# Optimization experiments

Measured on AMD Instinct MI355X. Metric: run time of the kernel, lower is better.

Reference implementation:

```python
import jax, jax.numpy as jnp
import numpy as np

NUM_INDUCING = 50
B = 1 << 20  # number of query states

Z_SCALE = jnp.array([0.25, 0.2, 0.08, 400.0, 10.0], dtype=jnp.float32)
Z_SHIFT = jnp.array([0.0, 0.0, 0.0, 800.0, 12.0], dtype=jnp.float32)


def setup_inputs() -> dict:
    key = jax.random.key(0)
    k1, k2 = jax.random.split(key)
    x_star = jax.random.normal(k1, (B, 5), dtype=jnp.float32)
    # learned params, faithful to the module's initializers
    log_lengthscale = jnp.log(jnp.array([0.2, 0.15, 0.1, 400.0, 15.0], dtype=jnp.float32))
    log_variance = jnp.asarray(jnp.log(0.08), dtype=jnp.float32)
    Z_raw = 0.5 * jax.random.normal(k2, (NUM_INDUCING, 5), dtype=jnp.float32)
    return {"x_star": x_star, "log_lengthscale": log_lengthscale,
            "log_variance": log_variance, "Z_raw": Z_raw}


def _matern52_from_d(d, prior_var):
    s = jnp.sqrt(5.0) * d
    return prior_var * (1.0 + s + (5.0 / 3.0) * d * d) * jnp.exp(-s)


def reference(x_star, log_lengthscale, log_variance, Z_raw):
    ls = jnp.exp(log_lengthscale)                      # (5,)
    prior_var = jnp.exp(log_variance)                  # scalar
    Z = jnp.tanh(Z_raw) * Z_SCALE + Z_SHIFT            # (M,5)
    inv_ls = 1.0 / (ls + 1e-8)
    Zs = Z * inv_ls                                    # scaled inducing pts (M,5)
    Xs = x_star * inv_ls                               # scaled queries (B,5)

    # K_ZZ: tiny (M,M), exact pairwise form
    diff = Zs[:, None, :] - Zs[None, :, :]             # (M,M,5)
    d_zz = jnp.sqrt(jnp.sum(diff * diff, axis=-1) + 1e-8)
    k_ZZ = _matern52_from_d(d_zz, prior_var)
    K_ZZ_inv = jnp.linalg.inv(k_ZZ + 1e-4 * jnp.eye(NUM_INDUCING, dtype=k_ZZ.dtype))

    # k_xZ: (B,M) via the GEMM-friendly expansion of squared distance
    x2 = jnp.sum(Xs * Xs, axis=-1)                     # (B,)
    z2 = jnp.sum(Zs * Zs, axis=-1)                     # (M,)
    d2 = x2[:, None] + z2[None, :] - 2.0 * (Xs @ Zs.T)  # (B,M)
    d_xz = jnp.sqrt(jnp.maximum(d2, 0.0) + 1e-8)
    k_xZ = _matern52_from_d(d_xz, prior_var)           # (B,M)

    red = jnp.einsum('bi,ij,bj->b', k_xZ, K_ZZ_inv, k_xZ)
    variance = jnp.maximum(prior_var - red, 1e-6)
    return jnp.sqrt(variance)                          # (B,)
```

## Files before the change

kernel.cpp:

```cpp
#include <hip/hip_runtime.h>
#include <hip/hip_bf16.h>
#include <math.h>

#define M 50
#define SQRT5 2.2360679774997896f

typedef short  bf16x8 __attribute__((ext_vector_type(8)));
typedef float  f32x4v __attribute__((ext_vector_type(4)));

__constant__ float c_zscale[5] = {0.25f, 0.2f, 0.08f, 400.0f, 10.0f};
__constant__ float c_zshift[5] = {0.0f, 0.0f, 0.0f, 800.0f, 12.0f};

#if __has_builtin(__builtin_amdgcn_sqrtf)
__device__ __forceinline__ float fsqrt(float x) { return __builtin_amdgcn_sqrtf(x); }
#else
__device__ __forceinline__ float fsqrt(float x) { return sqrtf(x); }
#endif

#if __has_builtin(__builtin_amdgcn_exp2f)
__device__ __forceinline__ float fexp2(float x) { return __builtin_amdgcn_exp2f(x); }
#else
__device__ __forceinline__ float fexp2(float x) { return exp2f(x); }
#endif

__device__ __forceinline__ float lane_bcast(float v, int lane) {
    return __builtin_bit_cast(float,
        __builtin_amdgcn_readlane(__builtin_bit_cast(int, v), lane));
}

__device__ __forceinline__ unsigned short bfu(float f) {
    return __builtin_bit_cast(unsigned short, __float2bfloat16(f));
}

#define FOR50(F) F(0) F(1) F(2) F(3) F(4) F(5) F(6) F(7) F(8) F(9) \
  F(10) F(11) F(12) F(13) F(14) F(15) F(16) F(17) F(18) F(19) \
  F(20) F(21) F(22) F(23) F(24) F(25) F(26) F(27) F(28) F(29) \
  F(30) F(31) F(32) F(33) F(34) F(35) F(36) F(37) F(38) F(39) \
  F(40) F(41) F(42) F(43) F(44) F(45) F(46) F(47) F(48) F(49)
#define FOR50P(F, p) F(0,p) F(1,p) F(2,p) F(3,p) F(4,p) F(5,p) F(6,p) F(7,p) F(8,p) F(9,p) \
  F(10,p) F(11,p) F(12,p) F(13,p) F(14,p) F(15,p) F(16,p) F(17,p) F(18,p) F(19,p) \
  F(20,p) F(21,p) F(22,p) F(23,p) F(24,p) F(25,p) F(26,p) F(27,p) F(28,p) F(29,p) \
  F(30,p) F(31,p) F(32,p) F(33,p) F(34,p) F(35,p) F(36,p) F(37,p) F(38,p) F(39,p) \
  F(40,p) F(41,p) F(42,p) F(43,p) F(44,p) F(45,p) F(46,p) F(47,p) F(48,p) F(49,p)

#define DECL_R(i) float r##i;
#define INIT_R(i) r##i = s_K[(i) * M + jc];
#define UPD(i, p) if ((i) != (p)) { \
    const float cp = lane_bcast(r##i, (p)); \
    r##i = fmaf(-cp, rowv, onp ? 0.0f : r##i); }
#define PIVOT(p) { \
    const float piv  = lane_bcast(r##p, (p)); \
    const float ipv  = 1.0f / piv; \
    const bool  onp  = (j == (p)); \
    const float rowv = onp ? ipv : r##p * ipv; \
    FOR50P(UPD, p) \
    r##p = rowv; }
#define WB_R(i) s_K[(i) * M + j] = r##i;

#define DECL_C(i) float c##i;
#define INIT_C(i) c##i = s_K[lrow * M + (i)];
#define CH_UPD(i, p) if ((i) > (p)) { \
    const float cj = lane_bcast(c##p, (i)); \
    c##i = fmaf(-c##p, cj, c##i); }
#define CH_PIVOT(p) { \
    const float dp  = lane_bcast(c##p, (p)); \
    const float inv = 1.0f / fsqrt(dp); \
    c##p *= inv; \
    FOR50P(CH_UPD, p) }
#define WB_C(i) if (t < M && (i) <= t) wtp[(i) * 64 + t] = bfu(pv * c##i);

__global__ __launch_bounds__(256, 1) void gp_setup(const float* __restrict__ log_ls,
                                                   const float* __restrict__ log_var,
                                                   const float* __restrict__ zraw,
                                                   float* __restrict__ ws) {
    __shared__ float s_ils[5];
    __shared__ float s_pv;
    __shared__ float s_Zs[M * 5];
    __shared__ float s_K[M * M];

    const int t = threadIdx.x;
    unsigned short* wtp = (unsigned short*)(ws + 512);

    if (t == 0) s_pv = expf(log_var[0]);
    if (t < 5)  s_ils[t] = 1.0f / (expf(log_ls[t]) + 1e-8f);
    __syncthreads();
    if (t < M * 5) {
        int j = t % 5;
        s_Zs[t] = (tanhf(zraw[t]) * c_zscale[j] + c_zshift[j]) * s_ils[j];
    }
    __syncthreads();
    const float pv = s_pv;

    for (int e = t; e < 4096; e += 256) wtp[e] = 0;
    for (int e = t; e < M * M; e += 256) {
        int i = e / M, jj = e % M;
        float d2 = 0.0f;
        #pragma unroll
        for (int q = 0; q < 5; ++q) {
            float df = s_Zs[i * 5 + q] - s_Zs[jj * 5 + q];
            d2 = fmaf(df, df, d2);
        }
        float d = fsqrt(d2 + 1e-8f);
        float s = SQRT5 * d;
        s_K[e] = pv * (1.0f + s + (5.0f / 3.0f) * (d * d)) * expf(-s)
                 + ((i == jj) ? 1e-4f : 0.0f);
    }
    __syncthreads();

    if (t < 64) {
        {
            const int j  = t;
            const int jc = (j < M) ? j : (M - 1);
            FOR50(DECL_R)
            FOR50(INIT_R)
            FOR50(PIVOT)
            if (j < M) { FOR50(WB_R) }
        }
        {
            const int lrow = (t < M) ? t : (M - 1);
            FOR50(DECL_C)
            FOR50(INIT_C)
            FOR50(CH_PIVOT)
            FOR50(WB_C)
        }
    }

    if (t < M * 5) ws[t] = -2.0f * SQRT5 * s_Zs[t];
    if (t < M) {
        float z2 = 0.0f;
        #pragma unroll
        for (int q = 0; q < 5; ++q) {
            float v = SQRT5 * s_Zs[t * 5 + q];
            z2 = fmaf(v, v, z2);
        }
        ws[256 + t] = z2 + 5e-8f;
    }
    if (t < 5)  ws[320 + t] = SQRT5 * s_ils[t];
    if (t == 0) ws[326] = pv;
}

__global__ __launch_bounds__(256) void gp_var(const float* __restrict__ x,
                                              const float* __restrict__ ws,
                                              float* __restrict__ out, int B) {
    __shared__ float sx[1280];
    __shared__ __align__(16) unsigned short sk[4 * 64 * 64];
    const int t    = threadIdx.x;
    const int lane = t & 63;
    const int wid  = t >> 6;
    const long long base = (long long)blockIdx.x * 1280;

    {
        const long long tot = (long long)B * 5;
        const float4* xv = (const float4*)(x + base);
        for (int i = t; i < 320; i += 256) {
            if (base + (long long)i * 4 + 3 < tot) ((float4*)sx)[i] = xv[i];
        }
    }
    __syncthreads();

    const float* __restrict__ Zb  = ws;
    const float* __restrict__ z2s = ws + 256;
    const float* __restrict__ ils = ws + 320;
    const float pv = ws[326];

    float xs[5];
    #pragma unroll
    for (int j = 0; j < 5; ++j) xs[j] = sx[t * 5 + j] * ils[j];

    float x2 = 0.0f;
    #pragma unroll
    for (int j = 0; j < 5; ++j) x2 = fmaf(xs[j], xs[j], x2);

    float k[M];
    #pragma unroll
    for (int m = 0; m < M; ++m) {
        float u = x2 + z2s[m];
        #pragma unroll
        for (int j = 0; j < 5; ++j) u = fmaf(Zb[m * 5 + j], xs[j], u);
        u = fmaxf(u, 5e-8f);
        float s = fsqrt(u);
        float e = fexp2(s * -1.4426950408889634f);
        k[m] = fmaf(u, (1.0f / 3.0f), 1.0f + s) * e;
    }

    char* kbase = (char*)sk + wid * 8192;
    const int swz_w = (lane & 7) << 4;
    #pragma unroll
    for (int c = 0; c < 8; ++c) {
        unsigned int w0, w1, w2, w3;
        #pragma unroll
        for (int q = 0; q < 4; ++q) {
            int kd0 = c * 8 + q * 2, kd1 = kd0 + 1;
            float f0 = (kd0 < M) ? k[kd0] : 0.0f;
            float f1 = (kd1 < M) ? k[kd1] : 0.0f;
            unsigned int wv = (unsigned int)bfu(f0) | ((unsigned int)bfu(f1) << 16);
            if (q == 0) w0 = wv; else if (q == 1) w1 = wv;
            else if (q == 2) w2 = wv; else w3 = wv;
        }
        int off = lane * 128 + ((c * 16) ^ swz_w);
        *(int4*)(kbase + off) = make_int4((int)w0, (int)w1, (int)w2, (int)w3);
    }

    const int r15 = lane & 15, g = lane >> 4;
    bf16x8 wf[4][2];
    const char* wtb = (const char*)(ws + 512);
    #pragma unroll
    for (int tc = 0; tc < 4; ++tc) {
        #pragma unroll
        for (int ks = 0; ks < 2; ++ks) {
            int o = ((tc * 16 + r15) * 64 + ks * 32 + g * 8) * 2;
            wf[tc][ks] = *(const bf16x8*)(wtb + o);
        }
    }

    float part[4][4];
    #pragma unroll
    for (int tr = 0; tr < 4; ++tr) {
        const int r = tr * 16 + r15;
        const char* arow = kbase + r * 128;
        const int swz = (r15 & 7) << 4;
        bf16x8 a0 = *(const bf16x8*)(arow + ((g * 16) ^ swz));
        bf16x8 a1 = *(const bf16x8*)(arow + (((4 + g) * 16) ^ swz));
        #pragma unroll
        for (int tc = 0; tc < 4; ++tc) {
            f32x4v acc = {0.0f, 0.0f, 0.0f, 0.0f};
            acc = __builtin_amdgcn_mfma_f32_16x16x32_bf16(a0, wf[tc][0], acc, 0, 0, 0);
            acc = __builtin_amdgcn_mfma_f32_16x16x32_bf16(a1, wf[tc][1], acc, 0, 0, 0);
            #pragma unroll
            for (int rg = 0; rg < 4; ++rg) {
                part[tr][rg] = (tc == 0) ? acc[rg] * acc[rg]
                                         : fmaf(acc[rg], acc[rg], part[tr][rg]);
            }
        }
    }

    #pragma unroll
    for (int tr = 0; tr < 4; ++tr) {
        #pragma unroll
        for (int rg = 0; rg < 4; ++rg) {
            float v = part[tr][rg];
            v += __shfl_xor(v, 1);
            v += __shfl_xor(v, 2);
            v += __shfl_xor(v, 4);
            v += __shfl_xor(v, 8);
            part[tr][rg] = v;
        }
    }

    float red = part[0][0];
    #pragma unroll
    for (int i = 1; i < 16; ++i)
        if (r15 == i) red = part[i >> 2][i & 3];

    const int pt = blockIdx.x * 256 + wid * 64 + (r15 >> 2) * 16 + g * 4 + (r15 & 3);
    out[pt] = fsqrt(fmaxf(pv - red, 1e-6f));
}

extern "C" void kernel_launch(void* const* d_in, const int* in_sizes, int n_in,
                              void* d_out, int out_size, void* d_ws, size_t ws_size,
                              hipStream_t stream) {
    const float* x    = (const float*)d_in[0];
    const float* ll   = (const float*)d_in[1];
    const float* lv   = (const float*)d_in[2];
    const float* zraw = (const float*)d_in[3];
    float* out = (float*)d_out;
    float* ws  = (float*)d_ws;

    const int B = in_sizes[0] / 5;

    hipLaunchKernelGGL(gp_setup, dim3(1), dim3(256), 0, stream, ll, lv, zraw, ws);
    const int grid = (B + 255) / 256;
    hipLaunchKernelGGL(gp_var, dim3(grid), dim3(256), 0, stream, x, ws, out, B);
}
```

Measured before the change: 72.72 us.

## Replace Gauss-Jordan inverse plus Cholesky with single Cholesky and triangular solve

The setup kernel used to invert K_ZZ by Gauss-Jordan and then Cholesky-factor the inverse to get the weight matrix. It now Cholesky-factors K_ZZ directly, writes L to shared memory, and computes L^{-1} by forward substitution per lane to emit the bf16 weights. This removes an entire 50-pivot elimination pass from the single-wave setup kernel and also uses a hardware reciprocal. The cost is a different factorization order with possibly different numerics, and the shared-memory reads in the solve loop.

```diff
diff --git a/kernel.cpp b/kernel.cpp
--- a/kernel.cpp
+++ b/kernel.cpp
@@ -21,6 +21,12 @@
 __device__ __forceinline__ float fexp2(float x) { return __builtin_amdgcn_exp2f(x); }
 #else
 __device__ __forceinline__ float fexp2(float x) { return exp2f(x); }
+#endif
+
+#if __has_builtin(__builtin_amdgcn_rcpf)
+__device__ __forceinline__ float frcp(float x) { return __builtin_amdgcn_rcpf(x); }
+#else
+__device__ __forceinline__ float frcp(float x) { return 1.0f / x; }
 #endif
 
 __device__ __forceinline__ float lane_bcast(float v, int lane) {
@@ -43,20 +49,6 @@
   F(30,p) F(31,p) F(32,p) F(33,p) F(34,p) F(35,p) F(36,p) F(37,p) F(38,p) F(39,p) \
   F(40,p) F(41,p) F(42,p) F(43,p) F(44,p) F(45,p) F(46,p) F(47,p) F(48,p) F(49,p)
 
-#define DECL_R(i) float r##i;
-#define INIT_R(i) r##i = s_K[(i) * M + jc];
-#define UPD(i, p) if ((i) != (p)) { \
-    const float cp = lane_bcast(r##i, (p)); \
-    r##i = fmaf(-cp, rowv, onp ? 0.0f : r##i); }
-#define PIVOT(p) { \
-    const float piv  = lane_bcast(r##p, (p)); \
-    const float ipv  = 1.0f / piv; \
-    const bool  onp  = (j == (p)); \
-    const float rowv = onp ? ipv : r##p * ipv; \
-    FOR50P(UPD, p) \
-    r##p = rowv; }
-#define WB_R(i) s_K[(i) * M + j] = r##i;
-
 #define DECL_C(i) float c##i;
 #define INIT_C(i) c##i = s_K[lrow * M + (i)];
 #define CH_UPD(i, p) if ((i) > (p)) { \
@@ -64,10 +56,19 @@
     c##i = fmaf(-c##p, cj, c##i); }
 #define CH_PIVOT(p) { \
     const float dp  = lane_bcast(c##p, (p)); \
-    const float inv = 1.0f / fsqrt(dp); \
+    const float inv = frcp(fsqrt(dp)); \
     c##p *= inv; \
+    if (lane < M) s_K[lane * M + (p)] = c##p; \
     FOR50P(CH_UPD, p) }
-#define WB_C(i) if (t < M && (i) <= t) wtp[(i) * 64 + t] = bfu(pv * c##i);
+
+#define DECL_Y(i) float y##i;
+#define TSU(q, i) if ((q) < (i)) acc = fmaf(-s_K[(i) * M + (q)], y##q, acc);
+#define TS_ROW(i) { \
+    float acc = (lane == (i)) ? 1.0f : 0.0f; \
+    FOR50P(TSU, i) \
+    y##i = acc * frcp(s_K[(i) * M + (i)]); }
+
+#define W_EMIT(i) wtp[(i) * 64 + lane] = bfu(pv * y##i);
 
 __global__ __launch_bounds__(256, 1) void gp_setup(const float* __restrict__ log_ls,
                                                    const float* __restrict__ log_var,
@@ -108,20 +109,17 @@
     __syncthreads();
 
     if (t < 64) {
+        const int lane = t;
+        const int lrow = (t < M) ? t : (M - 1);
         {
-            const int j  = t;
-            const int jc = (j < M) ? j : (M - 1);
-            FOR50(DECL_R)
-            FOR50(INIT_R)
-            FOR50(PIVOT)
-            if (j < M) { FOR50(WB_R) }
-        }
-        {
-            const int lrow = (t < M) ? t : (M - 1);
             FOR50(DECL_C)
             FOR50(INIT_C)
             FOR50(CH_PIVOT)
-            FOR50(WB_C)
+        }
+        {
+            FOR50(DECL_Y)
+            FOR50(TS_ROW)
+            FOR50(W_EMIT)
         }
     }
 
```

Result: faster. 60.08 us (-17.4%).
